# Optimization experiments

Measured on AMD Instinct MI355X. Metric: run time of the kernel, lower is better.

The kernel has to match this reference:

```python
import jax, jax.numpy as jnp
import numpy as np
from jax import lax

EPS = 1e-5
CLIP = 1.3  # Hardtanh(-1.3, 1.3)


def hardtanh(v):
    return jnp.clip(v, -CLIP, CLIP)


def binarize(v):
    # sign() forward with straight-through (identity) gradient, as in BCNN BinarizeF
    return v + lax.stop_gradient(jnp.sign(v) - v)


def bc_conv(x, w):
    # binarized conv: binarize both activations and weights, 3x3, stride 1, pad 1
    return lax.conv_general_dilated(
        binarize(x), binarize(w),
        window_strides=(1, 1), padding=((1, 1), (1, 1)),
        dimension_numbers=("NCHW", "OIHW", "NCHW"))


def batchnorm(v, gamma, beta):
    # batch statistics over (N, H, W), per-channel affine (DC_Bn4 variant)
    mean = jnp.mean(v, axis=(0, 2, 3), keepdims=True)
    var = jnp.var(v, axis=(0, 2, 3), keepdims=True)
    inv = lax.rsqrt(var + EPS)
    return (v - mean) * inv * gamma[None, :, None, None] + beta[None, :, None, None]


def setup_inputs() -> dict:
    key = jax.random.key(0)
    k_x, k_w1, k_w2 = jax.random.split(key, 3)
    C = 32
    x = jax.random.normal(k_x, (16, C, 224, 224), dtype=jnp.float32)
    w1 = jax.random.normal(k_w1, (C, C, 3, 3), dtype=jnp.float32) * 0.1
    w2 = jax.random.normal(k_w2, (C, C, 3, 3), dtype=jnp.float32) * 0.1
    g1 = jnp.ones((C,), jnp.float32); b1 = jnp.zeros((C,), jnp.float32)
    g2 = jnp.ones((C,), jnp.float32); b2 = jnp.zeros((C,), jnp.float32)
    return {"x": x, "w1": w1, "g1": g1, "b1": b1, "w2": w2, "g2": g2, "b2": b2}


def reference(x, w1, g1, b1, w2, g2, b2):
    y = batchnorm(bc_conv(hardtanh(x), w1), g1, b1)
    y = batchnorm(bc_conv(hardtanh(y), w2), g2, b2)
    return x + y
```

## Files before the change

kernel.cpp:

```cpp
#include <hip/hip_runtime.h>
#include <stdint.h>

#define NB 16
#define CC 32
#define HH 224
#define WW 224
#define HWP (HH*WW)
#define NHWP (NB*HWP)
#define PW 226
#define PSZ (PW*PW)

#define OFF_S1   0u
#define OFF_S2   3268864u
#define OFF_WP1  6537728u
#define OFF_WP2  6538880u
#define OFF_SQ1  6540032u
#define OFF_SQ2  6544128u
#define OFF_SUM1 6548224u
#define OFF_SUM2 6550272u

typedef int v4i    __attribute__((ext_vector_type(4)));
typedef int i32x16 __attribute__((ext_vector_type(16)));

__global__ void __launch_bounds__(256) k_setup(const uint32_t* __restrict__ w1,
                                               const uint32_t* __restrict__ w2,
                                               char* __restrict__ ws) {
    int t = blockIdx.x * 256 + threadIdx.x;
    if (t < 576) {
        const uint32_t* w = (t < 288) ? w1 : w2;
        uint32_t* o = (uint32_t*)(ws + ((t < 288) ? OFF_WP1 : OFF_WP2));
        int idx = (t < 288) ? t : t - 288;
        int oc = idx / 9, k = idx - oc * 9;
        uint32_t word = 0;
        for (int i = 0; i < 32; ++i)
            word |= (w[(oc * 32 + i) * 9 + k] >> 31) << i;
        o[idx] = word;
    } else if (t < 3648) {
        ((uint32_t*)(ws + OFF_SQ1))[t - 576] = 0u;
    } else if (t >= 4096 && t < 4096 + 28800) {
        int b = t - 4096;
        uint32_t* buf = (uint32_t*)(ws + ((b < 14400) ? OFF_S1 : OFF_S2));
        int bb = (b < 14400) ? b : b - 14400;
        int n = bb / 900;
        int e = bb - n * 900;
        int row, col;
        if (e < 226)      { row = 0;   col = e; }
        else if (e < 452) { row = 225; col = e - 226; }
        else { int k = e - 452; row = 1 + (k >> 1); col = (k & 1) ? 225 : 0; }
        buf[(size_t)n * PSZ + row * PW + col] = 0u;
    }
}

__global__ void __launch_bounds__(256) k_packx(const uint32_t* __restrict__ x,
                                               uint32_t* __restrict__ sp) {
    int t = blockIdx.x * 256 + threadIdx.x;
    int n = t / (HWP / 4);
    int rem4 = t - n * (HWP / 4);
    int px0 = rem4 * 4;
    int r = px0 / WW;
    int cw0 = px0 - r * WW;
    const uint32_t* xp = x + (size_t)n * CC * HWP + px0;
    uint32_t w0 = 0, w1 = 0, w2 = 0, w3 = 0;
    #pragma unroll
    for (int c = 0; c < 32; ++c) {
        uint4 v = *reinterpret_cast<const uint4*>(xp + (size_t)c * HWP);
        w0 |= (v.x >> 31) << c;
        w1 |= (v.y >> 31) << c;
        w2 |= (v.z >> 31) << c;
        w3 |= (v.w >> 31) << c;
    }
    uint32_t* op = sp + (size_t)n * PSZ + (r + 1) * PW + (cw0 + 1);
    op[0] = w0; op[1] = w1; op[2] = w2; op[3] = w3;
}

#define ASTRIDE 48
#define AROW (226*ASTRIDE)

__device__ __forceinline__ uint32_t spread4(uint32_t nib) {
    uint32_t s = (nib & 1u) | ((nib & 2u) << 7) | ((nib & 4u) << 14) | ((nib & 8u) << 21);
    return 0x01010101u ^ (s * 0xFEu);
}

__device__ __forceinline__ i32x16 conv_mfma(const uint32_t* __restrict__ sp,
                                            const uint32_t* __restrict__ wp,
                                            int n, int r, char* At) {
    for (int s = threadIdx.x; s < 3 * 226; s += 448) {
        int dr = s / 226, cc = s - dr * 226;
        int srow = r - 1 + dr, scol = cc - 1;
        uint32_t d8[8];
        if (srow < 0 || srow >= HH || scol < 0 || scol >= WW) {
            #pragma unroll
            for (int i = 0; i < 8; ++i) d8[i] = 0u;
        } else {
            uint32_t w = sp[(size_t)n * PSZ + (srow + 1) * PW + (scol + 1)];
            #pragma unroll
            for (int i = 0; i < 8; ++i) d8[i] = spread4((w >> (4 * i)) & 0xFu);
        }
        uint32_t* p = (uint32_t*)(At + s * ASTRIDE);
        *(uint4*)(p)     = make_uint4(d8[0], d8[1], d8[2], d8[3]);
        *(uint4*)(p + 4) = make_uint4(d8[4], d8[5], d8[6], d8[7]);
    }

    int l = threadIdx.x & 63;
    int oc = l & 31, kb = (l >> 5) * 16;
    v4i bf[9];
    #pragma unroll
    for (int t = 0; t < 9; ++t) {
        uint32_t w = wp[oc * 9 + t];
        uint32_t r0 = spread4((w >> (kb))      & 0xFu);
        uint32_t r1 = spread4((w >> (kb + 4))  & 0xFu);
        uint32_t r2 = spread4((w >> (kb + 8))  & 0xFu);
        uint32_t r3 = spread4((w >> (kb + 12)) & 0xFu);
        bf[t] = v4i{(int)r0, (int)r1, (int)r2, (int)r3};
    }
    __syncthreads();

    int wavebase = (threadIdx.x >> 6) * 32;
    int base = (wavebase + (l & 31)) * ASTRIDE + (l >> 5) * 16;

    i32x16 acc = {0,0,0,0,0,0,0,0,0,0,0,0,0,0,0,0};
    #pragma unroll
    for (int dh = 0; dh < 3; ++dh) {
        #pragma unroll
        for (int dw = 0; dw < 3; ++dw) {
            v4i a = *reinterpret_cast<const v4i*>(At + base + dh * AROW + dw * ASTRIDE);
            acc = __builtin_amdgcn_mfma_i32_32x32x32_i8(a, bf[dh * 3 + dw], acc, 0, 0, 0);
        }
    }
    return acc;
}

__global__ void __launch_bounds__(448) k_stats(const uint32_t* __restrict__ sp,
                                               const uint32_t* __restrict__ wp,
                                               int* __restrict__ g_sum,
                                               unsigned long long* __restrict__ g_sq) {
    __shared__ __align__(16) char At[3 * 226 * ASTRIDE];
    __shared__ int ls[7][32], lq[7][32];

    int n = blockIdx.x / HH, r = blockIdx.x - n * HH;
    i32x16 acc = conv_mfma(sp, wp, n, r, At);

    int l = threadIdx.x & 63;
    int s = 0, q = 0;
    #pragma unroll
    for (int g = 0; g < 16; ++g) { int c = acc[g]; s += c; q += c * c; }
    s += __shfl_xor(s, 32, 64);
    q += __shfl_xor(q, 32, 64);
    int wid = threadIdx.x >> 6;
    if (l < 32) { ls[wid][l] = s; lq[wid][l] = q; }
    __syncthreads();
    if (threadIdx.x < 32) {
        int S = 0, Q = 0;
        #pragma unroll
        for (int w = 0; w < 7; ++w) { S += ls[w][threadIdx.x]; Q += lq[w][threadIdx.x]; }
        int bin = blockIdx.x & 15;
        atomicAdd(&g_sum[bin * 32 + threadIdx.x], S);
        atomicAdd(&g_sq[bin * 32 + threadIdx.x], (unsigned long long)(long long)Q);
    }
}

__device__ __forceinline__ void build_affine16(const int* __restrict__ g_sum,
                                               const unsigned long long* __restrict__ g_sq,
                                               const float* __restrict__ gamma,
                                               const float* __restrict__ beta,
                                               float* aL, float* dL) {
    if (threadIdx.x < 32) {
        int c = threadIdx.x;
        int Si = 0; unsigned long long Qu = 0;
        #pragma unroll
        for (int b = 0; b < 16; ++b) { Si += g_sum[b * 32 + c]; Qu += g_sq[b * 32 + c]; }
        double M = (double)NHWP;
        double mean = (double)Si / M;
        double ex2 = (double)(long long)Qu / M;
        double var = ex2 - mean * mean;
        double inv = 1.0 / sqrt(var + 1e-5);
        double aa = inv * (double)gamma[c];
        aL[c] = (float)aa;
        dL[c] = (float)((double)beta[c] - aa * mean);
    }
}

__global__ void __launch_bounds__(448) k_sign(const uint32_t* __restrict__ sp,
                                              const uint32_t* __restrict__ wp,
                                              const int* __restrict__ g_sum,
                                              const unsigned long long* __restrict__ g_sq,
                                              const float* __restrict__ gamma,
                                              const float* __restrict__ beta,
                                              uint32_t* __restrict__ op) {
    __shared__ __align__(16) char At[3 * 226 * ASTRIDE];
    __shared__ float aL[32], dL[32];
    build_affine16(g_sum, g_sq, gamma, beta, aL, dL);

    int n = blockIdx.x / HH, r = blockIdx.x - n * HH;
    i32x16 acc = conv_mfma(sp, wp, n, r, At);

    int l = threadIdx.x & 63;
    int wavebase = (threadIdx.x >> 6) * 32;
    float a = aL[l & 31], d = dL[l & 31];
    uint32_t* orow = op + (size_t)n * PSZ + (r + 1) * PW + 1 + wavebase;
    #pragma unroll
    for (int g = 0; g < 16; ++g) {
        float y = fmaf(a, (float)acc[g], d);
        unsigned long long b = __ballot((__float_as_uint(y) >> 31) != 0u);
        if (l == 0) {
            int pxr = (g & 3) + 8 * (g >> 2);
            orow[pxr]     = (uint32_t)b;
            orow[pxr + 4] = (uint32_t)(b >> 32);
        }
    }
}

__device__ __forceinline__ void stage_lds(const uint32_t* __restrict__ wp,
                                          uint32_t (*Wl)[12], int (*Ctab)[32]) {
    for (int i = threadIdx.x; i < 288; i += 256) {
        int oc = i / 9, k = i - oc * 9;
        Wl[oc][k] = wp[i];
    }
    for (int i = threadIdx.x; i < 512; i += 256) {
        int ty = i >> 5, oc = i & 31;
        int s = 0;
        #pragma unroll
        for (int t = 0; t < 9; ++t) {
            int dh = t / 3 - 1, dw = t % 3 - 1;
            bool pad = ((ty & 1) && dh < 0) || ((ty & 2) && dh > 0) ||
                       ((ty & 4) && dw < 0) || ((ty & 8) && dw > 0);
            if (pad) s += 32 - 2 * __popc(wp[oc * 9 + t]);
        }
        Ctab[ty][oc] = s;
    }
}

__device__ __forceinline__ void decode_grp(int t, int& n, int& r, int& cw0) {
    n = t / 12544;
    int rem = t - n * 12544;
    r = rem / 56;
    cw0 = (rem - r * 56) * 4;
}

#define LOAD_TAPS18(base)                                                        \
    uint32_t u0 = (base)[-PW-1], u1 = (base)[-PW],   u2 = (base)[-PW+1],         \
             u3 = (base)[-PW+2], u4 = (base)[-PW+3], u5 = (base)[-PW+4];         \
    uint32_t m0 = (base)[-1],    m1 = (base)[0],     m2 = (base)[1],             \
             m3 = (base)[2],     m4 = (base)[3],     m5 = (base)[4];             \
    uint32_t l0 = (base)[PW-1],  l1 = (base)[PW],    l2 = (base)[PW+1],          \
             l3 = (base)[PW+2],  l4 = (base)[PW+3],  l5 = (base)[PW+4];

#define CONV4L(oc_)                                                              \
    int ocl = (oc_);                                                             \
    asm volatile("" : "+v"(ocl));                                                \
    const uint32_t* wr = &Wl[ocl][0];                                            \
    uint32_t w0 = wr[0], w1 = wr[1], w2 = wr[2], w3 = wr[3], w4 = wr[4],         \
             w5 = wr[5], w6 = wr[6], w7 = wr[7], w8 = wr[8];                     \
    int pc0 = __popc(u0^w0)+__popc(u1^w1)+__popc(u2^w2)                          \
            + __popc(m0^w3)+__popc(m1^w4)+__popc(m2^w5)                          \
            + __popc(l0^w6)+__popc(l1^w7)+__popc(l2^w8);                         \
    int pc1 = __popc(u1^w0)+__popc(u2^w1)+__popc(u3^w2)                          \
            + __popc(m1^w3)+__popc(m2^w4)+__popc(m3^w5)                          \
            + __popc(l1^w6)+__popc(l2^w7)+__popc(l3^w8);                         \
    int pc2 = __popc(u2^w0)+__popc(u3^w1)+__popc(u4^w2)                          \
            + __popc(m2^w3)+__popc(m3^w4)+__popc(m4^w5)                          \
            + __popc(l2^w6)+__popc(l3^w7)+__popc(l4^w8);                         \
    int pc3 = __popc(u3^w0)+__popc(u4^w1)+__popc(u5^w2)                          \
            + __popc(m3^w3)+__popc(m4^w4)+__popc(m5^w5)                          \
            + __popc(l3^w6)+__popc(l4^w7)+__popc(l5^w8);                         \
    int c0 = 288 - 2*pc0 - Ctab[ty0][ocl];                                       \
    int c1 = 288 - 2*pc1 - Ctab[rb][ocl];                                        \
    int c2 = 288 - 2*pc2 - Ctab[rb][ocl];                                        \
    int c3 = 288 - 2*pc3 - Ctab[ty3][ocl];

#define DECODE_BORDER()                                                          \
    int rb = (r == 0) ? 1 : (r == HH - 1) ? 2 : 0;                               \
    int ty0 = rb | ((cw0 == 0) ? 4 : 0);                                         \
    int ty3 = rb | ((cw0 == WW - 4) ? 8 : 0);

__global__ void __launch_bounds__(256) k_res(const uint32_t* __restrict__ sp,
                                             const uint32_t* __restrict__ wp,
                                             const int* __restrict__ g_sum,
                                             const unsigned long long* __restrict__ g_sq,
                                             const float* __restrict__ gamma,
                                             const float* __restrict__ beta,
                                             const float* __restrict__ x,
                                             float* __restrict__ out) {
    __shared__ __align__(16) uint32_t Wl[32][12];
    __shared__ int Ctab[16][32];
    __shared__ float aL[32], dL[32];
    stage_lds(wp, Wl, Ctab);
    build_affine16(g_sum, g_sq, gamma, beta, aL, dL);
    __syncthreads();

    int t = blockIdx.x * 256 + threadIdx.x;
    int n, r, cw0; decode_grp(t, n, r, cw0);
    const uint32_t* base = sp + (size_t)n * PSZ + (r + 1) * PW + (cw0 + 1);
    LOAD_TAPS18(base)
    DECODE_BORDER()

    size_t pix = (size_t)n * CC * HWP + (size_t)r * WW + cw0;
    #pragma unroll
    for (int oc = 0; oc < 32; ++oc) {
        CONV4L(oc)
        float a = aL[ocl], d = dL[ocl];
        float4 xv = *reinterpret_cast<const float4*>(x + pix + (size_t)ocl * HWP);
        float4 ov;
        ov.x = xv.x + fmaf(a, (float)c0, d);
        ov.y = xv.y + fmaf(a, (float)c1, d);
        ov.z = xv.z + fmaf(a, (float)c2, d);
        ov.w = xv.w + fmaf(a, (float)c3, d);
        *reinterpret_cast<float4*>(out + pix + (size_t)ocl * HWP) = ov;
    }
}

extern "C" void kernel_launch(void* const* d_in, const int* in_sizes, int n_in,
                              void* d_out, int out_size, void* d_ws, size_t ws_size,
                              hipStream_t stream) {
    const float* x  = (const float*)d_in[0];
    const float* w1 = (const float*)d_in[1];
    const float* g1 = (const float*)d_in[2];
    const float* b1 = (const float*)d_in[3];
    const float* w2 = (const float*)d_in[4];
    const float* g2 = (const float*)d_in[5];
    const float* b2 = (const float*)d_in[6];
    float* out = (float*)d_out;

    char* ws = (char*)d_ws;
    uint32_t* s1  = (uint32_t*)(ws + OFF_S1);
    uint32_t* s2  = (uint32_t*)(ws + OFF_S2);
    uint32_t* wp1 = (uint32_t*)(ws + OFF_WP1);
    uint32_t* wp2 = (uint32_t*)(ws + OFF_WP2);
    unsigned long long* sq1 = (unsigned long long*)(ws + OFF_SQ1);
    unsigned long long* sq2 = (unsigned long long*)(ws + OFF_SQ2);
    int* sum1 = (int*)(ws + OFF_SUM1);
    int* sum2 = (int*)(ws + OFF_SUM2);

    k_setup<<<132, 256, 0, stream>>>((const uint32_t*)w1, (const uint32_t*)w2, ws);
    k_packx<<<784, 256, 0, stream>>>((const uint32_t*)x, s1);
    k_stats<<<3584, 448, 0, stream>>>(s1, wp1, sum1, sq1);
    k_sign <<<3584, 448, 0, stream>>>(s1, wp1, sum1, sq1, g1, b1, s2);
    k_stats<<<3584, 448, 0, stream>>>(s2, wp2, sum2, sq2);
    k_res  <<<784, 256, 0, stream>>>(s2, wp2, sum2, sq2, g2, b2, x, out);
}
```

Before: 320.1 us.

## Precompute MFMA weight fragments and port residual kernel to int8 MFMA conv

The setup kernel now builds the ±1 int8 B-operand fragments for both layers once and stores them in the workspace. The conv kernels then load these fragments directly instead of unpacking the packed sign bits in every block. The final residual kernel drops its XOR/popcount bit-serial convolution with its border-correction table. It reuses the same LDS-staged MFMA path as the stats/sign kernels, one block per image row, fusing the BN affine and the residual add into the accumulator epilogue. This trades scalar popcount ALU work for matrix-core work, at the cost of re-staging activation rows through LDS and changing the output write pattern.

```diff
diff --git a/kernel.cpp b/kernel.cpp
--- a/kernel.cpp
+++ b/kernel.cpp
@@ -18,6 +18,8 @@
 #define OFF_SQ2  6544128u
 #define OFF_SUM1 6548224u
 #define OFF_SUM2 6550272u
+#define OFF_BF1  6552320u
+#define OFF_BF2  6561536u
 
 typedef int v4i    __attribute__((ext_vector_type(4)));
 typedef int i32x16 __attribute__((ext_vector_type(16)));
@@ -37,7 +39,7 @@
         o[idx] = word;
     } else if (t < 3648) {
         ((uint32_t*)(ws + OFF_SQ1))[t - 576] = 0u;
-    } else if (t >= 4096 && t < 4096 + 28800) {
+    } else if (t >= 4096 && t < 32896) {
         int b = t - 4096;
         uint32_t* buf = (uint32_t*)(ws + ((b < 14400) ? OFF_S1 : OFF_S2));
         int bb = (b < 14400) ? b : b - 14400;
@@ -48,6 +50,25 @@
         else if (e < 452) { row = 225; col = e - 226; }
         else { int k = e - 452; row = 1 + (k >> 1); col = (k & 1) ? 225 : 0; }
         buf[(size_t)n * PSZ + row * PW + col] = 0u;
+    } else if (t >= 32896 && t < 34048) {
+        int idx = t - 32896;
+        int layer = idx / 576, rem = idx - layer * 576;
+        int tap = rem / 64, lane = rem - tap * 64;
+        int oc = lane & 31, kb = (lane >> 5) * 16;
+        const uint32_t* w = layer ? w2 : w1;
+        uint32_t dw[4];
+        #pragma unroll
+        for (int d = 0; d < 4; ++d) {
+            uint32_t v = 0x01010101u;
+            #pragma unroll
+            for (int b = 0; b < 4; ++b) {
+                uint32_t sgn = w[(oc * 32 + kb + 4 * d + b) * 9 + tap] >> 31;
+                v ^= (0xFEu * sgn) << (8 * b);
+            }
+            dw[d] = v;
+        }
+        uint4* o = (uint4*)(ws + (layer ? OFF_BF2 : OFF_BF1));
+        o[tap * 64 + lane] = make_uint4(dw[0], dw[1], dw[2], dw[3]);
     }
 }
 
@@ -82,7 +103,7 @@
 }
 
 __device__ __forceinline__ i32x16 conv_mfma(const uint32_t* __restrict__ sp,
-                                            const uint32_t* __restrict__ wp,
+                                            const v4i* __restrict__ bfp,
                                             int n, int r, char* At) {
     for (int s = threadIdx.x; s < 3 * 226; s += 448) {
         int dr = s / 226, cc = s - dr * 226;
@@ -102,17 +123,9 @@
     }
 
     int l = threadIdx.x & 63;
-    int oc = l & 31, kb = (l >> 5) * 16;
     v4i bf[9];
     #pragma unroll
-    for (int t = 0; t < 9; ++t) {
-        uint32_t w = wp[oc * 9 + t];
-        uint32_t r0 = spread4((w >> (kb))      & 0xFu);
-        uint32_t r1 = spread4((w >> (kb + 4))  & 0xFu);
-        uint32_t r2 = spread4((w >> (kb + 8))  & 0xFu);
-        uint32_t r3 = spread4((w >> (kb + 12)) & 0xFu);
-        bf[t] = v4i{(int)r0, (int)r1, (int)r2, (int)r3};
-    }
+    for (int t = 0; t < 9; ++t) bf[t] = bfp[t * 64 + l];
     __syncthreads();
 
     int wavebase = (threadIdx.x >> 6) * 32;
@@ -131,14 +144,14 @@
 }
 
 __global__ void __launch_bounds__(448) k_stats(const uint32_t* __restrict__ sp,
-                                               const uint32_t* __restrict__ wp,
+                                               const v4i* __restrict__ bfp,
                                                int* __restrict__ g_sum,
                                                unsigned long long* __restrict__ g_sq) {
     __shared__ __align__(16) char At[3 * 226 * ASTRIDE];
     __shared__ int ls[7][32], lq[7][32];
 
     int n = blockIdx.x / HH, r = blockIdx.x - n * HH;
-    i32x16 acc = conv_mfma(sp, wp, n, r, At);
+    i32x16 acc = conv_mfma(sp, bfp, n, r, At);
 
     int l = threadIdx.x & 63;
     int s = 0, q = 0;
@@ -181,7 +194,7 @@
 }
 
 __global__ void __launch_bounds__(448) k_sign(const uint32_t* __restrict__ sp,
-                                              const uint32_t* __restrict__ wp,
+                                              const v4i* __restrict__ bfp,
                                               const int* __restrict__ g_sum,
                                               const unsigned long long* __restrict__ g_sq,
                                               const float* __restrict__ gamma,
@@ -192,7 +205,7 @@
     build_affine16(g_sum, g_sq, gamma, beta, aL, dL);
 
     int n = blockIdx.x / HH, r = blockIdx.x - n * HH;
-    i32x16 acc = conv_mfma(sp, wp, n, r, At);
+    i32x16 acc = conv_mfma(sp, bfp, n, r, At);
 
     int l = threadIdx.x & 63;
     int wavebase = (threadIdx.x >> 6) * 32;
@@ -210,102 +223,36 @@
     }
 }
 
-__device__ __forceinline__ void stage_lds(const uint32_t* __restrict__ wp,
-                                          uint32_t (*Wl)[12], int (*Ctab)[32]) {
-    for (int i = threadIdx.x; i < 288; i += 256) {
-        int oc = i / 9, k = i - oc * 9;
-        Wl[oc][k] = wp[i];
-    }
-    for (int i = threadIdx.x; i < 512; i += 256) {
-        int ty = i >> 5, oc = i & 31;
-        int s = 0;
-        #pragma unroll
-        for (int t = 0; t < 9; ++t) {
-            int dh = t / 3 - 1, dw = t % 3 - 1;
-            bool pad = ((ty & 1) && dh < 0) || ((ty & 2) && dh > 0) ||
-                       ((ty & 4) && dw < 0) || ((ty & 8) && dw > 0);
-            if (pad) s += 32 - 2 * __popc(wp[oc * 9 + t]);
-        }
-        Ctab[ty][oc] = s;
-    }
-}
-
-__device__ __forceinline__ void decode_grp(int t, int& n, int& r, int& cw0) {
-    n = t / 12544;
-    int rem = t - n * 12544;
-    r = rem / 56;
-    cw0 = (rem - r * 56) * 4;
-}
-
-#define LOAD_TAPS18(base)                                                        \
-    uint32_t u0 = (base)[-PW-1], u1 = (base)[-PW],   u2 = (base)[-PW+1],         \
-             u3 = (base)[-PW+2], u4 = (base)[-PW+3], u5 = (base)[-PW+4];         \
-    uint32_t m0 = (base)[-1],    m1 = (base)[0],     m2 = (base)[1],             \
-             m3 = (base)[2],     m4 = (base)[3],     m5 = (base)[4];             \
-    uint32_t l0 = (base)[PW-1],  l1 = (base)[PW],    l2 = (base)[PW+1],          \
-             l3 = (base)[PW+2],  l4 = (base)[PW+3],  l5 = (base)[PW+4];
-
-#define CONV4L(oc_)                                                              \
-    int ocl = (oc_);                                                             \
-    asm volatile("" : "+v"(ocl));                                                \
-    const uint32_t* wr = &Wl[ocl][0];                                            \
-    uint32_t w0 = wr[0], w1 = wr[1], w2 = wr[2], w3 = wr[3], w4 = wr[4],         \
-             w5 = wr[5], w6 = wr[6], w7 = wr[7], w8 = wr[8];                     \
-    int pc0 = __popc(u0^w0)+__popc(u1^w1)+__popc(u2^w2)                          \
-            + __popc(m0^w3)+__popc(m1^w4)+__popc(m2^w5)                          \
-            + __popc(l0^w6)+__popc(l1^w7)+__popc(l2^w8);                         \
-    int pc1 = __popc(u1^w0)+__popc(u2^w1)+__popc(u3^w2)                          \
-            + __popc(m1^w3)+__popc(m2^w4)+__popc(m3^w5)                          \
-            + __popc(l1^w6)+__popc(l2^w7)+__popc(l3^w8);                         \
-    int pc2 = __popc(u2^w0)+__popc(u3^w1)+__popc(u4^w2)                          \
-            + __popc(m2^w3)+__popc(m3^w4)+__popc(m4^w5)                          \
-            + __popc(l2^w6)+__popc(l3^w7)+__popc(l4^w8);                         \
-    int pc3 = __popc(u3^w0)+__popc(u4^w1)+__popc(u5^w2)                          \
-            + __popc(m3^w3)+__popc(m4^w4)+__popc(m5^w5)                          \
-            + __popc(l3^w6)+__popc(l4^w7)+__popc(l5^w8);                         \
-    int c0 = 288 - 2*pc0 - Ctab[ty0][ocl];                                       \
-    int c1 = 288 - 2*pc1 - Ctab[rb][ocl];                                        \
-    int c2 = 288 - 2*pc2 - Ctab[rb][ocl];                                        \
-    int c3 = 288 - 2*pc3 - Ctab[ty3][ocl];
-
-#define DECODE_BORDER()                                                          \
-    int rb = (r == 0) ? 1 : (r == HH - 1) ? 2 : 0;                               \
-    int ty0 = rb | ((cw0 == 0) ? 4 : 0);                                         \
-    int ty3 = rb | ((cw0 == WW - 4) ? 8 : 0);
-
-__global__ void __launch_bounds__(256) k_res(const uint32_t* __restrict__ sp,
-                                             const uint32_t* __restrict__ wp,
+__global__ void __launch_bounds__(448) k_res(const uint32_t* __restrict__ sp,
+                                             const v4i* __restrict__ bfp,
                                              const int* __restrict__ g_sum,
                                              const unsigned long long* __restrict__ g_sq,
                                              const float* __restrict__ gamma,
                                              const float* __restrict__ beta,
                                              const float* __restrict__ x,
                                              float* __restrict__ out) {
-    __shared__ __align__(16) uint32_t Wl[32][12];
-    __shared__ int Ctab[16][32];
+    __shared__ __align__(16) char At[3 * 226 * ASTRIDE];
     __shared__ float aL[32], dL[32];
-    stage_lds(wp, Wl, Ctab);
     build_affine16(g_sum, g_sq, gamma, beta, aL, dL);
-    __syncthreads();
-
-    int t = blockIdx.x * 256 + threadIdx.x;
-    int n, r, cw0; decode_grp(t, n, r, cw0);
-    const uint32_t* base = sp + (size_t)n * PSZ + (r + 1) * PW + (cw0 + 1);
-    LOAD_TAPS18(base)
-    DECODE_BORDER()
-
-    size_t pix = (size_t)n * CC * HWP + (size_t)r * WW + cw0;
-    #pragma unroll
-    for (int oc = 0; oc < 32; ++oc) {
-        CONV4L(oc)
-        float a = aL[ocl], d = dL[ocl];
-        float4 xv = *reinterpret_cast<const float4*>(x + pix + (size_t)ocl * HWP);
+
+    int n = blockIdx.x / HH, r = blockIdx.x - n * HH;
+    i32x16 acc = conv_mfma(sp, bfp, n, r, At);
+
+    int l = threadIdx.x & 63;
+    int oc = l & 31, hi = l >> 5;
+    int wavebase = (threadIdx.x >> 6) * 32;
+    float a = aL[oc], d = dL[oc];
+    size_t rowoff = (size_t)n * CC * HWP + (size_t)oc * HWP + (size_t)r * WW;
+    #pragma unroll
+    for (int g = 0; g < 4; ++g) {
+        int px0 = wavebase + 8 * g + 4 * hi;
+        float4 xv = *reinterpret_cast<const float4*>(x + rowoff + px0);
         float4 ov;
-        ov.x = xv.x + fmaf(a, (float)c0, d);
-        ov.y = xv.y + fmaf(a, (float)c1, d);
-        ov.z = xv.z + fmaf(a, (float)c2, d);
-        ov.w = xv.w + fmaf(a, (float)c3, d);
-        *reinterpret_cast<float4*>(out + pix + (size_t)ocl * HWP) = ov;
+        ov.x = xv.x + fmaf(a, (float)acc[4 * g + 0], d);
+        ov.y = xv.y + fmaf(a, (float)acc[4 * g + 1], d);
+        ov.z = xv.z + fmaf(a, (float)acc[4 * g + 2], d);
+        ov.w = xv.w + fmaf(a, (float)acc[4 * g + 3], d);
+        *reinterpret_cast<float4*>(out + rowoff + px0) = ov;
     }
 }
 
@@ -324,17 +271,17 @@
     char* ws = (char*)d_ws;
     uint32_t* s1  = (uint32_t*)(ws + OFF_S1);
     uint32_t* s2  = (uint32_t*)(ws + OFF_S2);
-    uint32_t* wp1 = (uint32_t*)(ws + OFF_WP1);
-    uint32_t* wp2 = (uint32_t*)(ws + OFF_WP2);
+    const v4i* bf1 = (const v4i*)(ws + OFF_BF1);
+    const v4i* bf2 = (const v4i*)(ws + OFF_BF2);
     unsigned long long* sq1 = (unsigned long long*)(ws + OFF_SQ1);
     unsigned long long* sq2 = (unsigned long long*)(ws + OFF_SQ2);
     int* sum1 = (int*)(ws + OFF_SUM1);
     int* sum2 = (int*)(ws + OFF_SUM2);
 
-    k_setup<<<132, 256, 0, stream>>>((const uint32_t*)w1, (const uint32_t*)w2, ws);
+    k_setup<<<134, 256, 0, stream>>>((const uint32_t*)w1, (const uint32_t*)w2, ws);
     k_packx<<<784, 256, 0, stream>>>((const uint32_t*)x, s1);
-    k_stats<<<3584, 448, 0, stream>>>(s1, wp1, sum1, sq1);
-    k_sign <<<3584, 448, 0, stream>>>(s1, wp1, sum1, sq1, g1, b1, s2);
-    k_stats<<<3584, 448, 0, stream>>>(s2, wp2, sum2, sq2);
-    k_res  <<<784, 256, 0, stream>>>(s2, wp2, sum2, sq2, g2, b2, x, out);
-}
+    k_stats<<<3584, 448, 0, stream>>>(s1, bf1, sum1, sq1);
+    k_sign <<<3584, 448, 0, stream>>>(s1, bf1, sum1, sq1, g1, b1, s2);
+    k_stats<<<3584, 448, 0, stream>>>(s2, bf2, sum2, sq2);
+    k_res  <<<3584, 448, 0, stream>>>(s2, bf2, sum2, sq2, g2, b2, x, out);
+}
```

Result: faster. 276.4 us (-13.7%).
